# Kernel optimization log

Measured on AMD Instinct MI355X. Metric: run time of the kernel, lower is better.

## Reference

```python
import jax, jax.numpy as jnp
import numpy as np

HEADS = 16
HEAD_DIM = 64
DIM = 1024
WH, WW = 32, 32
ROPE_DIM = 32  # = HEAD_DIM // 2
ROPE_BASE = 10000
EPS = 1e-6


def _rope_cache():
    # theta: [ROPE_DIM//2]
    theta = 1.0 / (ROPE_BASE ** (jnp.arange(0, ROPE_DIM, 2, dtype=jnp.float32)[: ROPE_DIM // 2] / ROPE_DIM))
    n = WH * WW
    idx = jnp.arange(n, dtype=jnp.float32)
    x_pos = idx % WW
    y_pos = idx // WW
    freqs = jnp.concatenate([x_pos[:, None] * theta[None, :], y_pos[:, None] * theta[None, :]], axis=-1)  # [n, ROPE_DIM]
    return jnp.cos(freqs), jnp.sin(freqs)


def _apply_rope(x, cos, sin):
    # x: [b, h, n, HEAD_DIM] -> pairs [b, h, n, ROPE_DIM, 2]
    xf = x.astype(jnp.float32).reshape(*x.shape[:-1], -1, 2)
    x0, x1 = xf[..., 0], xf[..., 1]
    c = cos[None, None, :, :]
    s = sin[None, None, :, :]
    out = jnp.stack([x0 * c - x1 * s, x1 * c + x0 * s], axis=-1)
    return out.reshape(*x.shape).astype(x.dtype)


def setup_inputs() -> dict:
    key = jax.random.key(0)
    ks = jax.random.split(key, 5)
    b, n = 16, WH * WW
    inner = HEADS * HEAD_DIM
    return {
        "x": jax.random.normal(ks[0], (b, n, DIM), dtype=jnp.float32),
        "t": jax.random.normal(ks[1], (b, DIM), dtype=jnp.float32),
        "norm_w": jnp.ones((DIM,), dtype=jnp.float32),
        "mod_w": jax.random.normal(ks[2], (2 * DIM, DIM), dtype=jnp.float32) * (DIM ** -0.5),
        "qkv_w": jax.random.normal(ks[3], (3 * inner, DIM), dtype=jnp.float32) * (DIM ** -0.5),
        "wo_w": jax.random.normal(ks[4], (DIM, inner), dtype=jnp.float32) * (inner ** -0.5),
    }


def reference(x, t, norm_w, mod_w, qkv_w, wo_w):
    b, n, dim = x.shape
    scale = HEAD_DIM ** -0.5

    # Modulated RMSNorm
    xf = x.astype(jnp.float32)
    xn = (xf * jax.lax.rsqrt(jnp.mean(xf * xf, axis=-1, keepdims=True) + EPS)).astype(x.dtype) * norm_w
    mod = t @ mod_w.T  # [b, 2*dim]
    sc, sh = mod[:, :dim], mod[:, dim:]
    h = xn * (1.0 + sc[:, None, :]) + sh[:, None, :]

    # QKV projection; rearrange 'b n (h d) -> b h n d' with d = 3*HEAD_DIM, THEN chunk
    qkv = h @ qkv_w.T  # [b, n, 3*inner]
    qkv = qkv.reshape(b, n, HEADS, 3 * HEAD_DIM).transpose(0, 2, 1, 3)  # [b, H, n, 3*hd]
    q, k, v = qkv[..., :HEAD_DIM], qkv[..., HEAD_DIM:2 * HEAD_DIM], qkv[..., 2 * HEAD_DIM:]

    # 2D axial RoPE on q, k
    cos, sin = _rope_cache()
    q = _apply_rope(q, cos, sin)
    k = _apply_rope(k, cos, sin)

    # SDPA (non-causal)
    attn = jax.nn.softmax(jnp.einsum('bhqd,bhkd->bhqk', q * scale, k), axis=-1)
    out = jnp.einsum('bhqk,bhkd->bhqd', attn, v)  # [b, H, n, hd]
    out = out.transpose(0, 2, 1, 3).reshape(b, n, HEADS * HEAD_DIM)
    return out @ wo_w.T
```

## Files before the change

### kernel.cpp

```cpp
#include <hip/hip_runtime.h>
#include <stdint.h>

typedef __bf16    bf16x8 __attribute__((ext_vector_type(8)));
typedef float     f32x4  __attribute__((ext_vector_type(4)));
typedef _Float16  f16;
typedef _Float16  f16x2  __attribute__((ext_vector_type(2)));
typedef _Float16  f16x4  __attribute__((ext_vector_type(4)));
typedef _Float16  f16x8  __attribute__((ext_vector_type(8)));

#define DEV __device__ __forceinline__

DEV ushort f2bf(float f) {
  union { float f; uint32_t u; } v; v.f = f;
  uint32_t u = v.u;
  return (ushort)((u + 0x7fffu + ((u >> 16) & 1u)) >> 16);
}

DEV f16x2 cvt_pkrtz(float a, float b) {
  return __builtin_bit_cast(f16x2, __builtin_amdgcn_cvt_pkrtz(a, b));
}

DEV void async16(const void* g, void* l) {
  __builtin_amdgcn_global_load_lds(
      (__attribute__((address_space(1))) void*)(uintptr_t)g,
      (__attribute__((address_space(3))) void*)(uint32_t)(uintptr_t)l,
      16, 0, 0);
}

__global__ __launch_bounds__(256)
void prep_kernel(const float* __restrict__ t, const float* __restrict__ mw,
                 float* __restrict__ mod,
                 const float* __restrict__ qkvw, ushort* __restrict__ wqk,
                 ushort* __restrict__ wv,
                 const float* __restrict__ wow, ushort* __restrict__ wowb) {
  const int id = blockIdx.x;
  const int tid = threadIdx.x;
  if (id < 2048) {
    const int j = id;
    const int w = tid >> 6, lane = tid & 63;
    float wr[16];
#pragma unroll
    for (int i = 0; i < 16; ++i) wr[i] = mw[(size_t)j * 1024 + lane + i * 64];
#pragma unroll
    for (int bb = 0; bb < 4; ++bb) {
      int b = w * 4 + bb;
      float s = 0.f;
#pragma unroll
      for (int i = 0; i < 16; ++i) s += wr[i] * t[b * 1024 + lane + i * 64];
#pragma unroll
      for (int m = 32; m >= 1; m >>= 1) s += __shfl_xor(s, m, 64);
      if (lane == 0) mod[b * 2048 + j] = s;
    }
  } else if (id < 5120) {
    const int j = id - 2048;
    uint32_t hd = (uint32_t)j / 192u;
    uint32_t rem = (uint32_t)j - hd * 192u;
    ushort* dst = (rem < 128u) ? (wqk + (size_t)(hd * 128u + rem) * 1024)
                               : (wv + (size_t)(hd * 64u + (rem - 128u)) * 1024);
    float4 v = ((const float4*)(qkvw + (size_t)j * 1024))[tid];
    ushort4 o;
    o.x = f2bf(v.x); o.y = f2bf(v.y); o.z = f2bf(v.z); o.w = f2bf(v.w);
    ((ushort4*)dst)[tid] = o;
  } else {
    const int i = (id - 5120) * 256 + tid;
    float4 v = ((const float4*)wow)[i];
    ushort4 o;
    o.x = f2bf(v.x); o.y = f2bf(v.y); o.z = f2bf(v.z); o.w = f2bf(v.w);
    ((ushort4*)wowb)[i] = o;
  }
}

__global__ __launch_bounds__(256)
void rms_mod_kernel(const float* __restrict__ x, const float* __restrict__ nw,
                    const float* __restrict__ mod, ushort* __restrict__ h) {
  int row = blockIdx.x;
  int b = row >> 10;
  int tid = threadIdx.x;
  const float4 xv = *(const float4*)(x + (size_t)row * 1024 + tid * 4);
  float ss = xv.x * xv.x + xv.y * xv.y + xv.z * xv.z + xv.w * xv.w;
#pragma unroll
  for (int m = 32; m >= 1; m >>= 1) ss += __shfl_xor(ss, m, 64);
  __shared__ float red[4];
  int w = tid >> 6, lane = tid & 63;
  if (lane == 0) red[w] = ss;
  __syncthreads();
  float tot = red[0] + red[1] + red[2] + red[3];
  float rn = rsqrtf(tot * (1.f / 1024.f) + 1e-6f);
  float4 wv = *(const float4*)(nw + tid * 4);
  float4 sc = *(const float4*)(mod + (size_t)b * 2048 + tid * 4);
  float4 sh = *(const float4*)(mod + (size_t)b * 2048 + 1024 + tid * 4);
  ushort4 o;
  o.x = f2bf(xv.x * rn * wv.x * (1.f + sc.x) + sh.x);
  o.y = f2bf(xv.y * rn * wv.y * (1.f + sc.y) + sh.y);
  o.z = f2bf(xv.z * rn * wv.z * (1.f + sc.z) + sh.z);
  o.w = f2bf(xv.w * rn * wv.w * (1.f + sc.w) + sh.w);
  *(ushort4*)(h + (size_t)row * 1024 + tid * 4) = o;
}

__global__ __launch_bounds__(256, 3)
void gemm_qkv_kernel(const ushort* __restrict__ hbuf, const ushort* __restrict__ wqk,
                     const ushort* __restrict__ wvw,
                     f16* __restrict__ qb, f16* __restrict__ kb,
                     f16* __restrict__ vtb) {
  __shared__ ushort smem[8192];
  ushort* As = smem;
  ushort* Bs = smem + 4096;
  const int K = 1024;
  const int id = blockIdx.x;
  int mode, m0, n0;
  const ushort *A, *B;
  if (id < 2048) {
    mode = 1; n0 = (id & 15) * 128; m0 = (id >> 4) * 128; A = hbuf; B = wqk;
  } else {
    int i2 = id - 2048;
    mode = 2; n0 = (i2 >> 3) * 128; m0 = (i2 & 7) * 128; A = wvw; B = hbuf;
  }
  const int tid = threadIdx.x;
  const int w = tid >> 6, lane = tid & 63, quad = lane >> 4, l15 = lane & 15;
  const int wm = (w >> 1) * 64, wn = (w & 1) * 64;
  const f32x4 fzero = {0.f, 0.f, 0.f, 0.f};
  f32x4 acc[4][4];
#pragma unroll
  for (int a = 0; a < 4; ++a)
#pragma unroll
    for (int b = 0; b < 4; ++b) acc[a][b] = fzero;

  const int s0 = tid, s1 = 256 + tid;
  const int r0 = s0 >> 2, c0 = (s0 & 3) ^ ((r0 >> 1) & 3);
  const int r1 = s1 >> 2, c1 = (s1 & 3) ^ ((r1 >> 1) & 3);
  const ushort* Ag0 = A + (size_t)(m0 + r0) * K + c0 * 8;
  const ushort* Ag1 = A + (size_t)(m0 + r1) * K + c1 * 8;
  const ushort* Bg0 = B + (size_t)(n0 + r0) * K + c0 * 8;
  const ushort* Bg1 = B + (size_t)(n0 + r1) * K + c1 * 8;

  for (int kt = 0; kt < K; kt += 32) {
    async16(Ag0 + kt, As + s0 * 8);
    async16(Ag1 + kt, As + s1 * 8);
    async16(Bg0 + kt, Bs + s0 * 8);
    async16(Bg1 + kt, Bs + s1 * 8);
    __syncthreads();
    bf16x8 af[4], bfr[4];
#pragma unroll
    for (int tm = 0; tm < 4; ++tm) {
      int r = wm + tm * 16 + l15;
      int cs = quad ^ ((r >> 1) & 3);
      af[tm] = *(const bf16x8*)(As + (r * 4 + cs) * 8);
    }
#pragma unroll
    for (int tn = 0; tn < 4; ++tn) {
      int r = wn + tn * 16 + l15;
      int cs = quad ^ ((r >> 1) & 3);
      bfr[tn] = *(const bf16x8*)(Bs + (r * 4 + cs) * 8);
    }
#pragma unroll
    for (int tm = 0; tm < 4; ++tm)
#pragma unroll
      for (int tn = 0; tn < 4; ++tn)
        acc[tm][tn] = __builtin_amdgcn_mfma_f32_16x16x32_bf16(af[tm], bfr[tn],
                                                              acc[tm][tn], 0, 0, 0);
    __syncthreads();
  }

  ushort* eps = smem + w * 2048;
  const int hd = (n0 + wn) >> 7, part = ((n0 + wn) >> 6) & 1;
  const float QS = part ? 1.f : 0.125f * 1.44269504f;
#pragma unroll
  for (int g = 0; g < 2; ++g) {
    __syncthreads();
#pragma unroll
    for (int ts = 0; ts < 2; ++ts) {
      int tm = g * 2 + ts;
#pragma unroll
      for (int tn = 0; tn < 4; ++tn)
#pragma unroll
        for (int r = 0; r < 4; ++r) {
          int row_loc = ts * 16 + quad * 4 + r;
          int col = tn * 16 + l15;
          int ch = (col >> 3) ^ (row_loc & 7);
          union { f16 h; ushort u; } cv;
          cv.h = (f16)acc[tm][tn][r];
          eps[row_loc * 64 + ch * 8 + (col & 7)] = cv.u;
        }
    }
    __syncthreads();
#pragma unroll
    for (int i = 0; i < 4; ++i) {
      int row_loc = i * 8 + (lane >> 3);
      int ch = lane & 7;
      union { uint4 u4; f16 h[8]; } uv;
      uv.u4 = *(const uint4*)(eps + row_loc * 64 + ((ch ^ (row_loc & 7)) * 8));
      int m = m0 + wm + g * 32 + row_loc;
      if (mode == 1) {
        int n = m & 1023;
#pragma unroll
        for (int t2 = 0; t2 < 4; ++t2) {
          int p = ch * 4 + t2;
          int jj = p & 15;
          float pos = (p < 16) ? (float)(n & 31) : (float)(n >> 5);
          float theta = __expf(-(float)jj * 0.5756462732485114f);
          float sn, cs;
          __sincosf(pos * theta, &sn, &cs);
          float x0 = (float)uv.h[2 * t2], x1 = (float)uv.h[2 * t2 + 1];
          f16x2 ro = cvt_pkrtz((x0 * cs - x1 * sn) * QS,
                               (x1 * cs + x0 * sn) * QS);
          uv.h[2 * t2] = ro[0];
          uv.h[2 * t2 + 1] = ro[1];
        }
        int b = m >> 10;
        ushort* dst = (ushort*)(part ? kb : qb) +
                      (((size_t)(b * 16 + hd) * 1024 + n) * 64 + ch * 8);
        *(uint4*)dst = uv.u4;
      } else {
        int b = (n0 + wn) >> 10, nn = (n0 + wn) & 1023;
        ushort* dst = (ushort*)vtb +
                      ((size_t)(b * 1024 + m) * 1024 + nn + ch * 8);
        *(uint4*)dst = uv.u4;
      }
    }
  }
}

__global__ __launch_bounds__(256, 3)
void gemm_wo_kernel(const ushort* __restrict__ A, const ushort* __restrict__ B,
                    float* __restrict__ outf) {
  __shared__ ushort smem[8192];
  ushort* As = smem;
  ushort* Bs = smem + 4096;
  const int K = 1024;
  const int m0 = blockIdx.y * 128, n0 = blockIdx.x * 128;
  const int tid = threadIdx.x;
  const int w = tid >> 6, lane = tid & 63, quad = lane >> 4, l15 = lane & 15;
  const int wm = (w >> 1) * 64, wn = (w & 1) * 64;
  const f32x4 fzero = {0.f, 0.f, 0.f, 0.f};
  f32x4 acc[4][4];
#pragma unroll
  for (int a = 0; a < 4; ++a)
#pragma unroll
    for (int b = 0; b < 4; ++b) acc[a][b] = fzero;

  const int s0 = tid, s1 = 256 + tid;
  const int r0 = s0 >> 2, c0 = (s0 & 3) ^ ((r0 >> 1) & 3);
  const int r1 = s1 >> 2, c1 = (s1 & 3) ^ ((r1 >> 1) & 3);
  const int b0 = m0 >> 10, nb = m0 & 1023;
  const size_t Abase = (size_t)b0 * 16 * 1024 * 64;
  const ushort* Ag0 = A + Abase + (size_t)(nb + r0) * 64 + c0 * 8;
  const ushort* Ag1 = A + Abase + (size_t)(nb + r1) * 64 + c1 * 8;
  const ushort* Bg0 = B + (size_t)(n0 + r0) * K + c0 * 8;
  const ushort* Bg1 = B + (size_t)(n0 + r1) * K + c1 * 8;

  for (int kt = 0; kt < K; kt += 32) {
    const size_t ka = (size_t)(kt >> 6) * 65536 + (size_t)(kt & 63);
    async16(Ag0 + ka, As + s0 * 8);
    async16(Ag1 + ka, As + s1 * 8);
    async16(Bg0 + kt, Bs + s0 * 8);
    async16(Bg1 + kt, Bs + s1 * 8);
    __syncthreads();
    bf16x8 af[4], bfr[4];
#pragma unroll
    for (int tm = 0; tm < 4; ++tm) {
      int r = wm + tm * 16 + l15;
      int cs = quad ^ ((r >> 1) & 3);
      af[tm] = *(const bf16x8*)(As + (r * 4 + cs) * 8);
    }
#pragma unroll
    for (int tn = 0; tn < 4; ++tn) {
      int r = wn + tn * 16 + l15;
      int cs = quad ^ ((r >> 1) & 3);
      bfr[tn] = *(const bf16x8*)(Bs + (r * 4 + cs) * 8);
    }
#pragma unroll
    for (int tm = 0; tm < 4; ++tm)
#pragma unroll
      for (int tn = 0; tn < 4; ++tn)
        acc[tm][tn] = __builtin_amdgcn_mfma_f32_16x16x32_bf16(af[tm], bfr[tn],
                                                              acc[tm][tn], 0, 0, 0);
    __syncthreads();
  }

#pragma unroll
  for (int tm = 0; tm < 4; ++tm)
#pragma unroll
    for (int tn = 0; tn < 4; ++tn) {
      int col = n0 + wn + tn * 16 + l15;
#pragma unroll
      for (int r = 0; r < 4; ++r) {
        int row = m0 + wm + tm * 16 + quad * 4 + r;
        outf[(size_t)row * 1024 + col] = acc[tm][tn][r];
      }
    }
}

__global__ __launch_bounds__(256, 3)
void attn_kernel(const f16* __restrict__ qbuf, const f16* __restrict__ kbuf,
                 const f16* __restrict__ vtbuf, ushort* __restrict__ aout) {
  __shared__ f16 Ks[128 * 64];
  __shared__ f16 Vs[64 * 128];

  const int id = blockIdx.x;
  const int xcd = id & 7, j = id >> 3;
  const int bh = xcd * 32 + (j >> 3);
  const int q0 = (j & 7) * 128;
  const f16* Qg = qbuf + (size_t)bh * 1024 * 64;
  const f16* Kg = kbuf + (size_t)bh * 1024 * 64;
  const f16* Vg = vtbuf + (size_t)bh * 64 * 1024;
  const int tid = threadIdx.x;
  const int w = tid >> 6, lane = tid & 63, quad = lane >> 4, l15 = lane & 15;
  const f32x4 fzero = {0.f, 0.f, 0.f, 0.f};

  f16x8 qf[2][2];
#pragma unroll
  for (int qs = 0; qs < 2; ++qs)
#pragma unroll
    for (int dc = 0; dc < 2; ++dc)
      qf[qs][dc] = *(const f16x8*)(Qg + (size_t)(q0 + w * 32 + qs * 16 + l15) * 64 +
                                   dc * 32 + quad * 8);

  f32x4 oacc[2][4];
#pragma unroll
  for (int qs = 0; qs < 2; ++qs)
#pragma unroll
    for (int ds = 0; ds < 4; ++ds) oacc[qs][ds] = fzero;
  float mrun[2] = {-1e30f, -1e30f}, lrun[2] = {0.f, 0.f};

  for (int kt = 0; kt < 1024; kt += 128) {
#pragma unroll
    for (int i = 0; i < 4; ++i) {
      int u = i * 256 + tid, r = u >> 3, c = u & 7;
      async16(Kg + (size_t)(kt + r) * 64 + (c ^ (r & 7)) * 8, Ks + u * 8);
    }
#pragma unroll
    for (int i = 0; i < 4; ++i) {
      int u = i * 256 + tid, r = u >> 4, c = u & 15;
      async16(Vg + (size_t)r * 1024 + kt + (c ^ (r & 15)) * 8, Vs + u * 8);
    }
    __syncthreads();

    f32x4 sacc[2][8];
#pragma unroll
    for (int qs = 0; qs < 2; ++qs)
#pragma unroll
      for (int ks = 0; ks < 8; ++ks) sacc[qs][ks] = fzero;
#pragma unroll
    for (int ks = 0; ks < 8; ++ks) {
#pragma unroll
      for (int dc = 0; dc < 2; ++dc) {
        int row = ks * 16 + l15;
        int ch = (dc * 4 + quad) ^ (row & 7);
        f16x8 kf = *(const f16x8*)(Ks + row * 64 + ch * 8);
        sacc[0][ks] = __builtin_amdgcn_mfma_f32_16x16x32_f16(kf, qf[0][dc], sacc[0][ks], 0, 0, 0);
        sacc[1][ks] = __builtin_amdgcn_mfma_f32_16x16x32_f16(kf, qf[1][dc], sacc[1][ks], 0, 0, 0);
      }
    }

    f16x4 pf[2][8];
#pragma unroll
    for (int qs = 0; qs < 2; ++qs) {
      const float* sv = (const float*)&sacc[qs][0];
      float mx = fmaxf(sv[0], sv[1]);
#pragma unroll
      for (int k = 2; k < 32; k += 2)
        mx = fmaxf(fmaxf(mx, sv[k]), sv[k + 1]);
      mx = fmaxf(mx, __shfl_xor(mx, 16, 64));
      mx = fmaxf(mx, __shfl_xor(mx, 32, 64));
      float mnew = fmaxf(mrun[qs], mx);
      float alpha = exp2f(mrun[qs] - mnew);
      mrun[qs] = mnew;
      float rs = 0.f;
#pragma unroll
      for (int ks = 0; ks < 8; ++ks) {
        float p0 = exp2f(sacc[qs][ks][0] - mnew);
        float p1 = exp2f(sacc[qs][ks][1] - mnew);
        float p2 = exp2f(sacc[qs][ks][2] - mnew);
        float p3 = exp2f(sacc[qs][ks][3] - mnew);
        rs += (p0 + p1) + (p2 + p3);
        union { f16x4 v; f16x2 h[2]; } pu;
        pu.h[0] = cvt_pkrtz(p0, p1);
        pu.h[1] = cvt_pkrtz(p2, p3);
        pf[qs][ks] = pu.v;
      }
      rs += __shfl_xor(rs, 16, 64);
      rs += __shfl_xor(rs, 32, 64);
      lrun[qs] = lrun[qs] * alpha + rs;
      float ar[4];
#pragma unroll
      for (int r = 0; r < 4; ++r) ar[r] = __shfl(alpha, quad * 4 + r, 64);
#pragma unroll
      for (int ds = 0; ds < 4; ++ds)
#pragma unroll
        for (int r = 0; r < 4; ++r) oacc[qs][ds][r] *= ar[r];
    }

#pragma unroll
    for (int ks = 0; ks < 8; ++ks) {
#pragma unroll
      for (int ds = 0; ds < 4; ++ds) {
        int row = ds * 16 + l15;
        int c16 = ks * 2 + (quad >> 1);
        f16x4 vf = *(const f16x4*)(Vs + row * 128 + ((c16 ^ (row & 15)) * 8) + (quad & 1) * 4);
        oacc[0][ds] = __builtin_amdgcn_mfma_f32_16x16x16f16(pf[0][ks], vf, oacc[0][ds], 0, 0, 0);
        oacc[1][ds] = __builtin_amdgcn_mfma_f32_16x16x16f16(pf[1][ks], vf, oacc[1][ds], 0, 0, 0);
      }
    }
    __syncthreads();
  }

  ushort* eps = (ushort*)Ks + w * 2048;
#pragma unroll
  for (int qs = 0; qs < 2; ++qs) {
    float linv[4];
#pragma unroll
    for (int r = 0; r < 4; ++r) linv[r] = 1.f / __shfl(lrun[qs], quad * 4 + r, 64);
#pragma unroll
    for (int ds = 0; ds < 4; ++ds)
#pragma unroll
      for (int r = 0; r < 4; ++r) {
        int row_loc = qs * 16 + quad * 4 + r;
        int col = ds * 16 + l15;
        int ch = (col >> 3) ^ (row_loc & 7);
        eps[row_loc * 64 + ch * 8 + (col & 7)] = f2bf(oacc[qs][ds][r] * linv[r]);
      }
  }
  __syncthreads();
  const size_t obase = ((size_t)bh * 1024 + q0 + w * 32) * 64;
#pragma unroll
  for (int i = 0; i < 4; ++i) {
    int row_loc = i * 8 + (lane >> 3);
    int ch = lane & 7;
    uint4 v = *(const uint4*)(eps + row_loc * 64 + ((ch ^ (row_loc & 7)) * 8));
    *(uint4*)(aout + obase + row_loc * 64 + ch * 8) = v;
  }
}

extern "C" void kernel_launch(void* const* d_in, const int* in_sizes, int n_in,
                              void* d_out, int out_size, void* d_ws, size_t ws_size,
                              hipStream_t stream) {
  const float* x    = (const float*)d_in[0];
  const float* t    = (const float*)d_in[1];
  const float* nw   = (const float*)d_in[2];
  const float* mw   = (const float*)d_in[3];
  const float* qkvw = (const float*)d_in[4];
  const float* wow  = (const float*)d_in[5];
  float* out = (float*)d_out;
  char* ws = (char*)d_ws;

  float*  modbuf  = (float*)(ws);
  ushort* hbuf    = (ushort*)(ws + 131072);
  ushort* wqk_b   = (ushort*)(ws + 33685504);
  ushort* wv_b    = (ushort*)(ws + 37879808);
  ushort* wow_b   = (ushort*)(ws + 39976960);
  f16*    qbuf    = (f16*)(ws + 42074112);
  f16*    kbuf    = (f16*)(ws + 75628544);
  f16*    vtbuf   = (f16*)(ws + 109182976);
  ushort* abuf    = (ushort*)(ws + 142737408);

  prep_kernel<<<dim3(6144), dim3(256), 0, stream>>>(
      t, mw, modbuf, qkvw, wqk_b, wv_b, wow, wow_b);
  rms_mod_kernel<<<dim3(16384), dim3(256), 0, stream>>>(x, nw, modbuf, hbuf);
  gemm_qkv_kernel<<<dim3(3072), dim3(256), 0, stream>>>(
      hbuf, wqk_b, wv_b, qbuf, kbuf, vtbuf);
  attn_kernel<<<dim3(2048), dim3(256), 0, stream>>>(qbuf, kbuf, vtbuf, abuf);
  gemm_wo_kernel<<<dim3(8, 128), dim3(256), 0, stream>>>(abuf, wow_b, out);
}
```

Before: 454.9 us.

## Rewrite QKV GEMM with 256x256 tiles, double-buffered LDS and interleaved staging

The QKV projection GEMM moves from 128x128 tiles with 256 threads to 256x256 tiles with 512 threads and a 64-wide K step. Global-to-LDS loads are double-buffered and split into four chunks issued between MFMA phases, with s_setprio raising wave priority during the MFMA phases. A block-index remap groups tiles across the grid. The epilogue hoists the RoPE theta computation out of the row loop. The aim is more operand reuse per LDS byte and overlap of memory traffic with matrix math. The cost is higher register and LDS pressure (128 KB LDS) and far fewer blocks in the grid.

```diff
diff --git a/kernel.cpp b/kernel.cpp
--- a/kernel.cpp
+++ b/kernel.cpp
@@ -97,125 +97,212 @@
   *(ushort4*)(h + (size_t)row * 1024 + tid * 4) = o;
 }
 
-__global__ __launch_bounds__(256, 3)
+__global__ __launch_bounds__(512, 2)
 void gemm_qkv_kernel(const ushort* __restrict__ hbuf, const ushort* __restrict__ wqk,
                      const ushort* __restrict__ wvw,
                      f16* __restrict__ qb, f16* __restrict__ kb,
                      f16* __restrict__ vtb) {
-  __shared__ ushort smem[8192];
-  ushort* As = smem;
-  ushort* Bs = smem + 4096;
-  const int K = 1024;
-  const int id = blockIdx.x;
+  __shared__ ushort smem[65536];
+  const int id0 = blockIdx.x;
+  const int id = (id0 & 7) * 96 + (id0 >> 3);
   int mode, m0, n0;
   const ushort *A, *B;
-  if (id < 2048) {
-    mode = 1; n0 = (id & 15) * 128; m0 = (id >> 4) * 128; A = hbuf; B = wqk;
+  if (id < 512) {
+    mode = 1; m0 = (id >> 3) * 256; n0 = (id & 7) * 256; A = hbuf; B = wqk;
   } else {
-    int i2 = id - 2048;
-    mode = 2; n0 = (i2 >> 3) * 128; m0 = (i2 & 7) * 128; A = wvw; B = hbuf;
+    const int i2 = id - 512;
+    mode = 2; n0 = (i2 >> 2) * 256; m0 = (i2 & 3) * 256; A = wvw; B = hbuf;
   }
   const int tid = threadIdx.x;
   const int w = tid >> 6, lane = tid & 63, quad = lane >> 4, l15 = lane & 15;
-  const int wm = (w >> 1) * 64, wn = (w & 1) * 64;
+  const int wm = w >> 2, wn = w & 3;
+
+  const int srow = tid >> 3;
+  const int sch  = (tid & 7) ^ (srow & 7);
+  const int soff = srow * 1024 + sch * 8;
+  const ushort* const Abase = A + (size_t)m0 * 1024;
+  const ushort* const Bbase = B + (size_t)n0 * 1024;
+  ushort* const As0 = smem;
+  ushort* const Bs0 = smem + 32768;
+  const int sdst = tid * 8;
+
+#define STG_A(d, t, h) do { \
+    async16(Abase + (h) * 131072 + soff + (t) * 64,          As0 + (d) * 16384 + (h) * 8192 + sdst); \
+    async16(Abase + (h) * 131072 + 65536 + soff + (t) * 64,  As0 + (d) * 16384 + (h) * 8192 + 4096 + sdst); } while (0)
+#define STG_B(d, t, h) do { \
+    async16(Bbase + (h) * 131072 + soff + (t) * 64,          Bs0 + (d) * 16384 + (h) * 8192 + sdst); \
+    async16(Bbase + (h) * 131072 + 65536 + soff + (t) * 64,  Bs0 + (d) * 16384 + (h) * 8192 + 4096 + sdst); } while (0)
+
+  int aoff[2], boff[2];
+#pragma unroll
+  for (int kk = 0; kk < 2; ++kk) {
+    const int swz = (((kk * 4 + quad) ^ (l15 & 7)) * 8);
+    aoff[kk] = (wm * 128 + l15) * 64 + swz;
+    boff[kk] = (wn * 64 + l15) * 64 + swz;
+  }
+
   const f32x4 fzero = {0.f, 0.f, 0.f, 0.f};
-  f32x4 acc[4][4];
-#pragma unroll
-  for (int a = 0; a < 4; ++a)
+  f32x4 acc[8][4];
+#pragma unroll
+  for (int a = 0; a < 8; ++a)
 #pragma unroll
     for (int b = 0; b < 4; ++b) acc[a][b] = fzero;
 
-  const int s0 = tid, s1 = 256 + tid;
-  const int r0 = s0 >> 2, c0 = (s0 & 3) ^ ((r0 >> 1) & 3);
-  const int r1 = s1 >> 2, c1 = (s1 & 3) ^ ((r1 >> 1) & 3);
-  const ushort* Ag0 = A + (size_t)(m0 + r0) * K + c0 * 8;
-  const ushort* Ag1 = A + (size_t)(m0 + r1) * K + c1 * 8;
-  const ushort* Bg0 = B + (size_t)(n0 + r0) * K + c0 * 8;
-  const ushort* Bg1 = B + (size_t)(n0 + r1) * K + c1 * 8;
-
-  for (int kt = 0; kt < K; kt += 32) {
-    async16(Ag0 + kt, As + s0 * 8);
-    async16(Ag1 + kt, As + s1 * 8);
-    async16(Bg0 + kt, Bs + s0 * 8);
-    async16(Bg1 + kt, Bs + s1 * 8);
-    __syncthreads();
-    bf16x8 af[4], bfr[4];
-#pragma unroll
-    for (int tm = 0; tm < 4; ++tm) {
-      int r = wm + tm * 16 + l15;
-      int cs = quad ^ ((r >> 1) & 3);
-      af[tm] = *(const bf16x8*)(As + (r * 4 + cs) * 8);
-    }
-#pragma unroll
-    for (int tn = 0; tn < 4; ++tn) {
-      int r = wn + tn * 16 + l15;
-      int cs = quad ^ ((r >> 1) & 3);
-      bfr[tn] = *(const bf16x8*)(Bs + (r * 4 + cs) * 8);
-    }
-#pragma unroll
-    for (int tm = 0; tm < 4; ++tm)
-#pragma unroll
-      for (int tn = 0; tn < 4; ++tn)
-        acc[tm][tn] = __builtin_amdgcn_mfma_f32_16x16x32_bf16(af[tm], bfr[tn],
-                                                              acc[tm][tn], 0, 0, 0);
-    __syncthreads();
-  }
-
-  ushort* eps = smem + w * 2048;
-  const int hd = (n0 + wn) >> 7, part = ((n0 + wn) >> 6) & 1;
-  const float QS = part ? 1.f : 0.125f * 1.44269504f;
-#pragma unroll
-  for (int g = 0; g < 2; ++g) {
-    __syncthreads();
-#pragma unroll
-    for (int ts = 0; ts < 2; ++ts) {
-      int tm = g * 2 + ts;
-#pragma unroll
-      for (int tn = 0; tn < 4; ++tn)
-#pragma unroll
-        for (int r = 0; r < 4; ++r) {
-          int row_loc = ts * 16 + quad * 4 + r;
-          int col = tn * 16 + l15;
-          int ch = (col >> 3) ^ (row_loc & 7);
-          union { f16 h; ushort u; } cv;
-          cv.h = (f16)acc[tm][tn][r];
-          eps[row_loc * 64 + ch * 8 + (col & 7)] = cv.u;
-        }
-    }
-    __syncthreads();
-#pragma unroll
-    for (int i = 0; i < 4; ++i) {
-      int row_loc = i * 8 + (lane >> 3);
-      int ch = lane & 7;
+  STG_A(0, 0, 0); STG_A(0, 0, 1); STG_B(0, 0, 0); STG_B(0, 0, 1);
+  asm volatile("s_waitcnt vmcnt(0)" ::: "memory");
+  __builtin_amdgcn_s_barrier();
+
+  bf16x8 af[4][2];
+  bf16x8 bfv[2][2];
+#pragma unroll 2
+  for (int t = 0; t < 16; ++t) {
+    const int cur = t & 1, nxt = cur ^ 1;
+    const int tn = (t < 15) ? t + 1 : 15;
+    const ushort* Asc = As0 + cur * 16384;
+    const ushort* Bsc = Bs0 + cur * 16384;
+
+#pragma unroll
+    for (int mf = 0; mf < 4; ++mf)
+#pragma unroll
+      for (int kk = 0; kk < 2; ++kk)
+        af[mf][kk] = *(const bf16x8*)(Asc + mf * 1024 + aoff[kk]);
+#pragma unroll
+    for (int nf = 0; nf < 2; ++nf)
+#pragma unroll
+      for (int kk = 0; kk < 2; ++kk)
+        bfv[nf][kk] = *(const bf16x8*)(Bsc + nf * 1024 + boff[kk]);
+    STG_A(nxt, tn, 0);
+    __builtin_amdgcn_s_barrier();
+    __builtin_amdgcn_s_setprio(1);
+#pragma unroll
+    for (int mf = 0; mf < 4; ++mf)
+#pragma unroll
+      for (int nf = 0; nf < 2; ++nf)
+#pragma unroll
+        for (int kk = 0; kk < 2; ++kk)
+          acc[mf][nf] = __builtin_amdgcn_mfma_f32_16x16x32_bf16(
+              af[mf][kk], bfv[nf][kk], acc[mf][nf], 0, 0, 0);
+    __builtin_amdgcn_s_setprio(0);
+    __builtin_amdgcn_s_barrier();
+
+#pragma unroll
+    for (int mf = 0; mf < 4; ++mf)
+#pragma unroll
+      for (int kk = 0; kk < 2; ++kk)
+        af[mf][kk] = *(const bf16x8*)(Asc + (4 + mf) * 1024 + aoff[kk]);
+    STG_A(nxt, tn, 1);
+    __builtin_amdgcn_s_barrier();
+    __builtin_amdgcn_s_setprio(1);
+#pragma unroll
+    for (int mf = 0; mf < 4; ++mf)
+#pragma unroll
+      for (int nf = 0; nf < 2; ++nf)
+#pragma unroll
+        for (int kk = 0; kk < 2; ++kk)
+          acc[4 + mf][nf] = __builtin_amdgcn_mfma_f32_16x16x32_bf16(
+              af[mf][kk], bfv[nf][kk], acc[4 + mf][nf], 0, 0, 0);
+    __builtin_amdgcn_s_setprio(0);
+    __builtin_amdgcn_s_barrier();
+
+#pragma unroll
+    for (int nf = 0; nf < 2; ++nf)
+#pragma unroll
+      for (int kk = 0; kk < 2; ++kk)
+        bfv[nf][kk] = *(const bf16x8*)(Bsc + (2 + nf) * 1024 + boff[kk]);
+    STG_B(nxt, tn, 0);
+    __builtin_amdgcn_s_barrier();
+    __builtin_amdgcn_s_setprio(1);
+#pragma unroll
+    for (int mf = 0; mf < 4; ++mf)
+#pragma unroll
+      for (int nf = 0; nf < 2; ++nf)
+#pragma unroll
+        for (int kk = 0; kk < 2; ++kk)
+          acc[4 + mf][2 + nf] = __builtin_amdgcn_mfma_f32_16x16x32_bf16(
+              af[mf][kk], bfv[nf][kk], acc[4 + mf][2 + nf], 0, 0, 0);
+    __builtin_amdgcn_s_setprio(0);
+    __builtin_amdgcn_s_barrier();
+
+#pragma unroll
+    for (int mf = 0; mf < 4; ++mf)
+#pragma unroll
+      for (int kk = 0; kk < 2; ++kk)
+        af[mf][kk] = *(const bf16x8*)(Asc + mf * 1024 + aoff[kk]);
+    STG_B(nxt, tn, 1);
+    __builtin_amdgcn_s_barrier();
+    __builtin_amdgcn_s_setprio(1);
+#pragma unroll
+    for (int mf = 0; mf < 4; ++mf)
+#pragma unroll
+      for (int nf = 0; nf < 2; ++nf)
+#pragma unroll
+        for (int kk = 0; kk < 2; ++kk)
+          acc[mf][2 + nf] = __builtin_amdgcn_mfma_f32_16x16x32_bf16(
+              af[mf][kk], bfv[nf][kk], acc[mf][2 + nf], 0, 0, 0);
+    __builtin_amdgcn_s_setprio(0);
+    asm volatile("s_waitcnt vmcnt(0)" ::: "memory");
+    __builtin_amdgcn_s_barrier();
+  }
+#undef STG_A
+#undef STG_B
+
+  ushort* eps = smem + w * 8192;
+#pragma unroll
+  for (int mf = 0; mf < 8; ++mf)
+#pragma unroll
+    for (int nf = 0; nf < 4; ++nf)
+#pragma unroll
+      for (int r = 0; r < 4; ++r) {
+        const int row_loc = mf * 16 + quad * 4 + r;
+        const int col = nf * 16 + l15;
+        const int ch = (col >> 3) ^ (row_loc & 7);
+        union { f16 h; ushort u; } cv;
+        cv.h = (f16)acc[mf][nf][r];
+        eps[row_loc * 64 + ch * 8 + (col & 7)] = cv.u;
+      }
+
+  const int ch = lane & 7;
+  const int rbase = lane >> 3;
+  const int gcol = n0 + wn * 64;
+  if (mode == 1) {
+    const int hd = gcol >> 7, part = (gcol >> 6) & 1;
+    const float QS = part ? 1.f : 0.125f * 1.44269504f;
+    f16* const outp = part ? kb : qb;
+    float th[4];
+#pragma unroll
+    for (int t2 = 0; t2 < 4; ++t2)
+      th[t2] = __expf(-(float)((ch * 4 + t2) & 15) * 0.5756462732485114f);
+#pragma unroll
+    for (int i = 0; i < 16; ++i) {
+      const int row_loc = i * 8 + rbase;
       union { uint4 u4; f16 h[8]; } uv;
       uv.u4 = *(const uint4*)(eps + row_loc * 64 + ((ch ^ (row_loc & 7)) * 8));
-      int m = m0 + wm + g * 32 + row_loc;
-      if (mode == 1) {
-        int n = m & 1023;
-#pragma unroll
-        for (int t2 = 0; t2 < 4; ++t2) {
-          int p = ch * 4 + t2;
-          int jj = p & 15;
-          float pos = (p < 16) ? (float)(n & 31) : (float)(n >> 5);
-          float theta = __expf(-(float)jj * 0.5756462732485114f);
-          float sn, cs;
-          __sincosf(pos * theta, &sn, &cs);
-          float x0 = (float)uv.h[2 * t2], x1 = (float)uv.h[2 * t2 + 1];
-          f16x2 ro = cvt_pkrtz((x0 * cs - x1 * sn) * QS,
-                               (x1 * cs + x0 * sn) * QS);
-          uv.h[2 * t2] = ro[0];
-          uv.h[2 * t2 + 1] = ro[1];
-        }
-        int b = m >> 10;
-        ushort* dst = (ushort*)(part ? kb : qb) +
-                      (((size_t)(b * 16 + hd) * 1024 + n) * 64 + ch * 8);
-        *(uint4*)dst = uv.u4;
-      } else {
-        int b = (n0 + wn) >> 10, nn = (n0 + wn) & 1023;
-        ushort* dst = (ushort*)vtb +
-                      ((size_t)(b * 1024 + m) * 1024 + nn + ch * 8);
-        *(uint4*)dst = uv.u4;
-      }
+      const int m = m0 + wm * 128 + row_loc;
+      const int n = m & 1023;
+      const float xpos = (float)(n & 31), ypos = (float)(n >> 5);
+#pragma unroll
+      for (int t2 = 0; t2 < 4; ++t2) {
+        const int p = ch * 4 + t2;
+        const float pos = (p < 16) ? xpos : ypos;
+        float sn, cs;
+        __sincosf(pos * th[t2], &sn, &cs);
+        const float x0 = (float)uv.h[2 * t2], x1 = (float)uv.h[2 * t2 + 1];
+        f16x2 ro = cvt_pkrtz((x0 * cs - x1 * sn) * QS, (x1 * cs + x0 * sn) * QS);
+        uv.h[2 * t2] = ro[0];
+        uv.h[2 * t2 + 1] = ro[1];
+      }
+      f16* dst = outp + (((size_t)((m >> 10) * 16 + hd) * 1024 + n) * 64 + ch * 8);
+      *(uint4*)dst = uv.u4;
+    }
+  } else {
+    const int b = gcol >> 10, tb = gcol & 1023;
+#pragma unroll
+    for (int i = 0; i < 16; ++i) {
+      const int row_loc = i * 8 + rbase;
+      const uint4 v = *(const uint4*)(eps + row_loc * 64 + ((ch ^ (row_loc & 7)) * 8));
+      const int m = m0 + wm * 128 + row_loc;
+      f16* dst = vtb + ((size_t)(b * 1024 + m) * 1024 + tb + ch * 8);
+      *(uint4*)dst = v;
     }
   }
 }
@@ -456,7 +543,7 @@
   prep_kernel<<<dim3(6144), dim3(256), 0, stream>>>(
       t, mw, modbuf, qkvw, wqk_b, wv_b, wow, wow_b);
   rms_mod_kernel<<<dim3(16384), dim3(256), 0, stream>>>(x, nw, modbuf, hbuf);
-  gemm_qkv_kernel<<<dim3(3072), dim3(256), 0, stream>>>(
+  gemm_qkv_kernel<<<dim3(768), dim3(512), 0, stream>>>(
       hbuf, wqk_b, wv_b, qbuf, kbuf, vtbuf);
   attn_kernel<<<dim3(2048), dim3(256), 0, stream>>>(qbuf, kbuf, vtbuf, abuf);
   gemm_wo_kernel<<<dim3(8, 128), dim3(256), 0, stream>>>(abuf, wow_b, out);
```

After: 437.4 us. 1.04x faster.
